# Kernel optimization log

Measured on AMD Instinct MI355X. Metric: run time of the kernel, lower is better.

The kernel has to match this reference:

```python
import jax, jax.numpy as jnp
import numpy as np

HG, WG, DG = 16, 16, 8   # bilateral grid size
NP = 12                  # affine params per pixel (3x4)
DS = 256                 # input_downsample


def _resize_bilinear(x, oh, ow):
    # torch F.interpolate(mode='bilinear', align_corners=False)
    B, C, H, W = x.shape
    sy, sx = H / oh, W / ow
    ys = jnp.clip((jnp.arange(oh, dtype=x.dtype) + 0.5) * sy - 0.5, 0.0, H - 1)
    xs = jnp.clip((jnp.arange(ow, dtype=x.dtype) + 0.5) * sx - 0.5, 0.0, W - 1)
    y0 = jnp.floor(ys).astype(jnp.int32); y1 = jnp.minimum(y0 + 1, H - 1)
    x0 = jnp.floor(xs).astype(jnp.int32); x1 = jnp.minimum(x0 + 1, W - 1)
    wy = (ys - y0.astype(x.dtype))[None, None, :, None]
    wx = (xs - x0.astype(x.dtype))[None, None, None, :]
    top = x[:, :, y0, :] * (1 - wy) + x[:, :, y1, :] * wy      # [B,C,oh,W]
    return top[:, :, :, x0] * (1 - wx) + top[:, :, :, x1] * wx  # [B,C,oh,ow]


def _conv(x, w, b):
    y = jax.lax.conv_general_dilated(x, w, (1, 1), 'SAME',
                                     dimension_numbers=('NCHW', 'OIHW', 'NCHW'))
    return y + b[None, :, None, None]


def _slice(grid, guide):
    # grid [B,C,Hg,Wg,D], guide [B,H,W] in [0,1].
    # Equivalent to the per-depth grid_sample(align_corners=True, border) +
    # depth gather/lerp loop: one fused trilinear lookup per pixel.
    B, C, Hg, Wg, D = grid.shape
    H, W = guide.shape[1], guide.shape[2]
    ys = jnp.arange(H, dtype=grid.dtype) * ((Hg - 1) / (H - 1))
    xs = jnp.arange(W, dtype=grid.dtype) * ((Wg - 1) / (W - 1))
    y0 = jnp.floor(ys).astype(jnp.int32); y1 = jnp.minimum(y0 + 1, Hg - 1)
    x0 = jnp.floor(xs).astype(jnp.int32); x1 = jnp.minimum(x0 + 1, Wg - 1)
    wy = (ys - y0.astype(grid.dtype))[:, None]   # [H,1]
    wx = (xs - x0.astype(grid.dtype))[None, :]   # [1,W]
    d = guide * (D - 1)
    d0 = jnp.clip(jnp.floor(d), 0, D - 1).astype(jnp.int32)
    d1 = jnp.minimum(d0 + 1, D - 1)
    wd = jnp.clip(d - d0.astype(grid.dtype), 0.0, 1.0)  # [B,H,W]

    Y0, Y1 = y0[:, None], y1[:, None]
    X0, X1 = x0[None, :], x1[None, :]

    def per_b(g, d0b, d1b, wdb):
        def dlerp(yi, xi):
            # g[:, yi, xi, d] -> [C,H,W]; lerp over depth
            return (1 - wdb) * g[:, yi, xi, d0b] + wdb * g[:, yi, xi, d1b]
        return ((1 - wy) * (1 - wx) * dlerp(Y0, X0)
                + (1 - wy) * wx * dlerp(Y0, X1)
                + wy * (1 - wx) * dlerp(Y1, X0)
                + wy * wx * dlerp(Y1, X1))

    return jax.vmap(per_b)(grid, d0, d1, wd)  # [B,C,H,W]


def _forward(x, w1, b1, w2, b2, w3, b3, w4, b4, w5, b5, w6, b6):
    B, C, H, W = x.shape
    guide = jnp.clip(0.299 * x[:, 0] + 0.587 * x[:, 1] + 0.114 * x[:, 2], 0.0, 1.0)
    scale = min(1.0, DS / max(H, W))
    if scale < 1.0:
        x_low = _resize_bilinear(x, int(H * scale), int(W * scale))
    else:
        x_low = x
    f = jax.nn.relu(_conv(x_low, w1, b1))
    f = jax.nn.relu(_conv(f, w2, b2))
    f = jax.nn.relu(_conv(f, w3, b3))
    c = jax.nn.relu(_conv(f, w4, b4))
    c = jax.nn.relu(_conv(c, w5, b5))
    c = _conv(c, w6, b6)                        # [B, NP*DG, H_low, W_low]
    c = _resize_bilinear(c, HG, WG)             # [B, NP*DG, HG, WG]
    grid = c.reshape(B, NP, DG, HG, WG).transpose(0, 1, 3, 4, 2)  # [B,NP,HG,WG,DG]
    sc = _slice(grid, guide)                    # [B, NP, H, W]
    co = sc.reshape(B, 3, 4, H, W)
    y = jnp.einsum('bijhw,bjhw->bihw', co[:, :, :3], x) + co[:, :, 3]
    return jnp.clip(y, 0.0, 1.0)


def setup_inputs() -> dict:
    key = jax.random.key(0)
    ks = jax.random.split(key, 7)
    x = jax.random.uniform(ks[0], (2, 3, 1024, 1024), dtype=jnp.float32)
    def wmat(k, o, i):
        return jax.random.normal(k, (o, i, 3, 3), jnp.float32) / np.sqrt(i * 9.0)
    return dict(
        x=x,
        w1=wmat(ks[1], 16, 3), b1=jnp.zeros((16,), jnp.float32),
        w2=wmat(ks[2], 32, 16), b2=jnp.zeros((32,), jnp.float32),
        w3=wmat(ks[3], 32, 32), b3=jnp.zeros((32,), jnp.float32),
        w4=wmat(ks[4], 64, 32), b4=jnp.zeros((64,), jnp.float32),
        w5=wmat(ks[5], 64, 64), b5=jnp.zeros((64,), jnp.float32),
        w6=wmat(ks[6], 96, 64), b6=jnp.zeros((96,), jnp.float32),
    )


def reference(x, w1, b1, w2, b2, w3, b3, w4, b4, w5, b5, w6, b6):
    return _forward(x, w1, b1, w2, b2, w3, b3, w4, b4, w5, b5, w6, b6)
```

## Files before the change

kernel.cpp:

```cpp
#include <hip/hip_runtime.h>
#include <hip/hip_bf16.h>

#define HW1K  1048576

typedef float  f4    __attribute__((ext_vector_type(4)));
typedef float  f32x4 __attribute__((ext_vector_type(4)));
typedef short  s16x8 __attribute__((ext_vector_type(8)));
typedef unsigned short u16x8 __attribute__((ext_vector_type(8)));

__device__ __forceinline__ float bf2f(unsigned short u) {
    unsigned int b = ((unsigned int)u) << 16;
    return __builtin_bit_cast(float, b);
}
__device__ __forceinline__ void fsplit(float x, unsigned short& h, unsigned short& l) {
    unsigned int xb = __builtin_bit_cast(unsigned int, x);
    h = (unsigned short)(xb >> 16);
    float fh = __builtin_bit_cast(float, xb & 0xffff0000u);
    float r = x - fh;
    l = (unsigned short)(__builtin_bit_cast(unsigned int, r) >> 16);
}

__global__ __launch_bounds__(256)
void prep_wM(const float* __restrict__ w2, const float* __restrict__ w3,
             const float* __restrict__ w4, const float* __restrict__ w5,
             const float* __restrict__ w6,
             unsigned short* __restrict__ Wh, unsigned short* __restrict__ Wl) {
    int i = blockIdx.x * 256 + threadIdx.x;
    if (i >= 124928) return;
    const float* src; int base, cin, kp_;
    if      (i < 5120)  { src = w2; base = 0;     cin = 16; kp_ = 160; }
    else if (i < 14336) { src = w3; base = 5120;  cin = 32; kp_ = 288; }
    else if (i < 32768) { src = w4; base = 14336; cin = 32; kp_ = 288; }
    else if (i < 69632) { src = w5; base = 32768; cin = 64; kp_ = 576; }
    else                { src = w6; base = 69632; cin = 64; kp_ = 576; }
    int r  = i - base;
    int co = r / kp_;
    int kp = r % kp_;
    int kk = kp / cin;
    int ci = kp % cin;
    float v = (kk < 9) ? src[(co * cin + ci) * 9 + kk] : 0.0f;
    unsigned short h, l; fsplit(v, h, l);
    Wh[i] = h; Wl[i] = l;
}

template <int WIN, int CIN, int COUT, int KP, int SO, int HOIST>
__device__ __forceinline__ void layerM(const unsigned short* sH, const unsigned short* sL,
                                       unsigned short* dH, unsigned short* dL,
                                       const unsigned short* __restrict__ Wh,
                                       const unsigned short* __restrict__ Wl,
                                       const float* __restrict__ bias) {
    constexpr int WOUT = WIN - 2;
    constexpr int NPX  = WOUT * WOUT;
    constexpr int CINP = CIN + 8;
    constexpr int MT   = (NPX + 15) / 16;
    constexpr int NT   = COUT / 16;
    constexpr int WPN  = 4 / NT;
    constexpr int KS   = KP / 32;

    const int wid  = threadIdx.x >> 6;
    const int lane = threadIdx.x & 63;
    const int m    = lane & 15;
    const int g    = lane >> 4;

    const int nt    = wid % NT;
    const int chunk = wid / NT;
    const int co    = nt * 16 + m;

    const unsigned short* wbh = Wh + (size_t)co * KP + 8 * g;
    const unsigned short* wbl = Wl + (size_t)co * KP + 8 * g;

    s16x8 bH[HOIST ? KS : 1], bL[HOIST ? KS : 1];
    if constexpr (HOIST) {
        #pragma unroll
        for (int k0 = 0; k0 < KS; ++k0) {
            bH[k0] = *(const s16x8*)(wbh + k0 * 32);
            bL[k0] = *(const s16x8*)(wbl + k0 * 32);
        }
    }
    const float bv = bias[co];

    #pragma unroll 1
    for (int mt = chunk; mt < MT; mt += WPN) {
        const int mt0 = mt * 16;
        int px = mt0 + m; if (px > NPX - 1) px = NPX - 1;
        const int pbase = (px / WOUT) * WIN + (px % WOUT);

        f32x4 aHH = {0,0,0,0}, aHL = {0,0,0,0}, aLH = {0,0,0,0};
        #pragma unroll
        for (int k0 = 0; k0 < KS; ++k0) {
            const int k   = k0 * 32 + 8 * g;
            const int kk  = k / CIN;
            const int ci0 = k % CIN;
            const int aoff = (pbase + (kk / 3) * WIN + (kk % 3)) * CINP + ci0;
            s16x8 avh = *(const s16x8*)(&sH[aoff]);
            s16x8 avl = *(const s16x8*)(&sL[aoff]);
            s16x8 bvh, bvl;
            if constexpr (HOIST) { bvh = bH[k0]; bvl = bL[k0]; }
            else {
                bvh = *(const s16x8*)(wbh + k0 * 32);
                bvl = *(const s16x8*)(wbl + k0 * 32);
            }
            aHH = __builtin_amdgcn_mfma_f32_16x16x32_bf16(avh, bvh, aHH, 0, 0, 0);
            aHL = __builtin_amdgcn_mfma_f32_16x16x32_bf16(avh, bvl, aHL, 0, 0, 0);
            aLH = __builtin_amdgcn_mfma_f32_16x16x32_bf16(avl, bvh, aLH, 0, 0, 0);
        }
        #pragma unroll
        for (int j = 0; j < 4; ++j) {
            int opx = mt0 + g * 4 + j;
            if (opx < NPX) {
                float v = fmaxf(aHH[j] + aHL[j] + aLH[j] + bv, 0.0f);
                unsigned short h, l; fsplit(v, h, l);
                dH[opx * SO + co] = h;
                dL[opx * SO + co] = l;
            }
        }
    }
}

__global__ __launch_bounds__(256, 3)
void fusedM(const float* __restrict__ x, const float* __restrict__ w1,
            const float* __restrict__ b1,
            const unsigned short* __restrict__ Wh, const unsigned short* __restrict__ Wl,
            const float* __restrict__ b2, const float* __restrict__ b3,
            const float* __restrict__ b4, const float* __restrict__ b5,
            unsigned short* __restrict__ P6h, unsigned short* __restrict__ P6l) {
    __shared__ float sC[592];
    __shared__ __align__(16) unsigned short AH[3840], AL[3840];
    __shared__ __align__(16) unsigned short BH[4000], BL[4000];

    const int cell = blockIdx.x;
    const int b = cell >> 8, gy = (cell >> 4) & 15, gx = cell & 15;

    for (int i = threadIdx.x; i < 588; i += 256) {
        int c = i / 196, t = i % 196;
        int xi = t % 14, yi = t / 14;
        int ya = 16 * gy + 1 + yi, xa = 16 * gx + 1 + xi;
        const float* p = x + ((size_t)(b * 3 + c)) * HW1K + (4 * ya + 1) * 1024 + (4 * xa + 1);
        sC[i] = 0.25f * (p[0] + p[1] + p[1024] + p[1025]);
    }
    for (int i = threadIdx.x; i < 384; i += 256) { AH[3456 + i] = 0; AL[3456 + i] = 0; }
    __syncthreads();

    {
        const int wid  = __builtin_amdgcn_readfirstlane(threadIdx.x >> 6);
        const int lane = threadIdx.x & 63;
        const int co0  = wid * 4;
        float acc[3][4]; int pxs[3], pb[3];
        #pragma unroll
        for (int t = 0; t < 3; ++t) {
            int px = lane + t * 64; if (px > 143) px = 143;
            pxs[t] = px; pb[t] = (px / 12) * 14 + (px % 12);
            #pragma unroll
            for (int j = 0; j < 4; ++j) acc[t][j] = b1[co0 + j];
        }
        for (int ci = 0; ci < 3; ++ci)
            #pragma unroll
            for (int k = 0; k < 9; ++k) {
                float w[4];
                #pragma unroll
                for (int j = 0; j < 4; ++j) w[j] = w1[((co0 + j) * 3 + ci) * 9 + k];
                const int ko = (k / 3) * 14 + (k % 3);
                #pragma unroll
                for (int t = 0; t < 3; ++t) {
                    float a = sC[ci * 196 + pb[t] + ko];
                    #pragma unroll
                    for (int j = 0; j < 4; ++j) acc[t][j] = fmaf(w[j], a, acc[t][j]);
                }
            }
        #pragma unroll
        for (int t = 0; t < 3; ++t)
            #pragma unroll
            for (int j = 0; j < 4; ++j) {
                float v = fmaxf(acc[t][j], 0.0f);
                unsigned short h, l; fsplit(v, h, l);
                AH[pxs[t] * 24 + co0 + j] = h;
                AL[pxs[t] * 24 + co0 + j] = l;
            }
    }
    __syncthreads();

    layerM<12, 16, 32, 160, 40, 1>(AH, AL, BH, BL, Wh + 0,     Wl + 0,     b2);
    __syncthreads();
    layerM<10, 32, 32, 288, 40, 1>(BH, BL, AH, AL, Wh + 5120,  Wl + 5120,  b3);
    __syncthreads();
    layerM< 8, 32, 64, 288, 72, 1>(AH, AL, BH, BL, Wh + 14336, Wl + 14336, b4);
    __syncthreads();
    layerM< 6, 64, 64, 576, 72, 0>(BH, BL, AH, AL, Wh + 32768, Wl + 32768, b5);
    __syncthreads();

    for (int t = threadIdx.x; t < 576; t += 256) {
        int kk = t >> 6, ci = t & 63;
        int ky = kk / 3, kx = kk % 3;
        float v = 0.0f;
        #pragma unroll
        for (int dr = 0; dr < 2; ++dr)
            #pragma unroll
            for (int dc = 0; dc < 2; ++dc) {
                int px = (ky + dr) * 4 + (kx + dc);
                v += bf2f(AH[px * 72 + ci]) + bf2f(AL[px * 72 + ci]);
            }
        v *= 0.25f;
        unsigned short h, l; fsplit(v, h, l);
        P6h[(size_t)cell * 576 + t] = h;
        P6l[(size_t)cell * 576 + t] = l;
    }
}

__global__ __launch_bounds__(64)
void gemm6(const unsigned short* __restrict__ Bh, const unsigned short* __restrict__ Bl,
           const unsigned short* __restrict__ W6h, const unsigned short* __restrict__ W6l,
           const float* __restrict__ b6, float* __restrict__ c16) {
    const int cell0 = blockIdx.x * 16;
    const int co0   = blockIdx.y * 16;
    const int lane  = threadIdx.x;
    const int m = lane & 15, g = lane >> 4;

    const unsigned short* pah = Bh  + (size_t)(cell0 + m) * 576 + 8 * g;
    const unsigned short* pal = Bl  + (size_t)(cell0 + m) * 576 + 8 * g;
    const unsigned short* pbh = W6h + (size_t)(co0 + m) * 576 + 8 * g;
    const unsigned short* pbl = W6l + (size_t)(co0 + m) * 576 + 8 * g;

    f32x4 aHH = {0,0,0,0}, aHL = {0,0,0,0}, aLH = {0,0,0,0};
    #pragma unroll 6
    for (int k0 = 0; k0 < 576; k0 += 32) {
        s16x8 avh = *(const s16x8*)(pah + k0);
        s16x8 avl = *(const s16x8*)(pal + k0);
        s16x8 bvh = *(const s16x8*)(pbh + k0);
        s16x8 bvl = *(const s16x8*)(pbl + k0);
        aHH = __builtin_amdgcn_mfma_f32_16x16x32_bf16(avh, bvh, aHH, 0, 0, 0);
        aHL = __builtin_amdgcn_mfma_f32_16x16x32_bf16(avh, bvl, aHL, 0, 0, 0);
        aLH = __builtin_amdgcn_mfma_f32_16x16x32_bf16(avl, bvh, aLH, 0, 0, 0);
    }
    const int co = co0 + m;
    const float bv = b6[co];
    #pragma unroll
    for (int j = 0; j < 4; ++j) {
        int cell = cell0 + g * 4 + j;
        float v = aHH[j] + aHL[j] + aLH[j] + bv;
        int b = cell >> 8, gyx = cell & 255;
        c16[(size_t)b * 24576 + (gyx * 8 + (co & 7)) * 12 + (co >> 3)] = v;
    }
}

__global__ __launch_bounds__(256)
void slice_apply4(const float* __restrict__ x, const float* __restrict__ c16,
                  float* __restrict__ out) {
    int t = blockIdx.x * 256 + threadIdx.x;
    int po4 = t * 4;
    int b   = po4 >> 20;
    int po  = po4 & (HW1K - 1);
    int py  = po >> 10;
    int px0 = po & 1023;

    const float* xb = x + (size_t)b * 3 * HW1K;
    f4 rv  = *(const f4*)(xb + po);
    f4 gv  = *(const f4*)(xb + HW1K + po);
    f4 bv  = *(const f4*)(xb + 2 * HW1K + po);

    float ysf = (float)py * (15.0f / 1023.0f);
    int y0 = (int)floorf(ysf); int y1 = min(y0 + 1, 15);
    float wy = ysf - (float)y0;

    const float* gb = c16 + (size_t)b * 24576;
    f4 outv[3];

    #pragma unroll
    for (int s = 0; s < 4; ++s) {
        float r  = rv[s], g = gv[s], bl = bv[s];
        int   px = px0 + s;

        float gd = fminf(fmaxf(0.299f * r + 0.587f * g + 0.114f * bl, 0.0f), 1.0f);

        float xsf = (float)px * (15.0f / 1023.0f);
        int x0 = (int)floorf(xsf); int x1 = min(x0 + 1, 15);
        float wx = xsf - (float)x0;

        float d  = gd * 7.0f;
        int d0 = (int)floorf(d); d0 = max(0, min(d0, 7));
        int d1 = min(d0 + 1, 7);
        float wd = fminf(fmaxf(d - (float)d0, 0.0f), 1.0f);

        float co[12];
        #pragma unroll
        for (int p = 0; p < 12; ++p) co[p] = 0.0f;

        #pragma unroll
        for (int cy = 0; cy < 2; ++cy) {
            int   yy  = cy ? y1 : y0;
            float wyf = cy ? wy : 1.0f - wy;
            #pragma unroll
            for (int cx = 0; cx < 2; ++cx) {
                int   xx  = cx ? x1 : x0;
                float wyx = wyf * (cx ? wx : 1.0f - wx);
                const float* g0 = gb + ((yy * 16 + xx) * 8 + d0) * 12;
                const float* g1 = gb + ((yy * 16 + xx) * 8 + d1) * 12;
                float wA = wyx * (1.0f - wd), wB = wyx * wd;
                #pragma unroll
                for (int p = 0; p < 12; ++p) co[p] += wA * g0[p] + wB * g1[p];
            }
        }

        #pragma unroll
        for (int i = 0; i < 3; ++i) {
            float v = co[i * 4 + 0] * r + co[i * 4 + 1] * g + co[i * 4 + 2] * bl + co[i * 4 + 3];
            outv[i][s] = fminf(fmaxf(v, 0.0f), 1.0f);
        }
    }

    float* ob = out + (size_t)b * 3 * HW1K;
    #pragma unroll
    for (int i = 0; i < 3; ++i)
        *(f4*)(ob + i * HW1K + po) = outv[i];
}

extern "C" void kernel_launch(void* const* d_in, const int* in_sizes, int n_in,
                              void* d_out, int out_size, void* d_ws, size_t ws_size,
                              hipStream_t stream) {
    const float* x  = (const float*)d_in[0];
    const float* w1 = (const float*)d_in[1];  const float* b1 = (const float*)d_in[2];
    const float* w2 = (const float*)d_in[3];  const float* b2 = (const float*)d_in[4];
    const float* w3 = (const float*)d_in[5];  const float* b3 = (const float*)d_in[6];
    const float* w4 = (const float*)d_in[7];  const float* b4 = (const float*)d_in[8];
    const float* w5 = (const float*)d_in[9];  const float* b5 = (const float*)d_in[10];
    const float* w6 = (const float*)d_in[11]; const float* b6 = (const float*)d_in[12];
    float* out = (float*)d_out;

    char* w = (char*)d_ws;
    unsigned short* Wh  = (unsigned short*)w;   w += 124928 * 2;
    unsigned short* Wl  = (unsigned short*)w;   w += 124928 * 2;
    unsigned short* P6h = (unsigned short*)w;   w += 512 * 576 * 2;
    unsigned short* P6l = (unsigned short*)w;   w += 512 * 576 * 2;
    float*          c16 = (float*)w;

    prep_wM<<<dim3(489),  dim3(256), 0, stream>>>(w2, w3, w4, w5, w6, Wh, Wl);
    fusedM <<<dim3(512),  dim3(256), 0, stream>>>(x, w1, b1, Wh, Wl, b2, b3, b4, b5, P6h, P6l);
    gemm6  <<<dim3(32, 6), dim3(64), 0, stream>>>(P6h, P6l, Wh + 69632, Wl + 69632, b6, c16);
    slice_apply4<<<dim3(2 * HW1K / 4 / 256), dim3(256), 0, stream>>>(x, c16, out);

    (void)in_sizes; (void)n_in; (void)out_size; (void)ws_size;
}
```

Baseline: 66.67 us.

## Double fusedM block to 512 threads, splitting layer work across 8 waves

Launches the fused conv kernel with 8 waves per block instead of 4, so each MFMA layer splits output tiles across twice as many waves (WPN doubled). The first conv layer is restructured so waves split pixel slices as well as output channels. This aims to hide latency within each of the 512 cells, since there are only 512 blocks. The cost is more register pressure per block (launch bounds become 512,2) and the extra waves may sit idle in small layers.

Result: slower. 71.73 us (+7.6%).

```diff
diff --git a/kernel.cpp b/kernel.cpp
--- a/kernel.cpp
+++ b/kernel.cpp
@@ -54,7 +54,7 @@
     constexpr int CINP = CIN + 8;
     constexpr int MT   = (NPX + 15) / 16;
     constexpr int NT   = COUT / 16;
-    constexpr int WPN  = 4 / NT;
+    constexpr int WPN  = 8 / NT;
     constexpr int KS   = KP / 32;
 
     const int wid  = threadIdx.x >> 6;
@@ -117,7 +117,7 @@
     }
 }
 
-__global__ __launch_bounds__(256, 3)
+__global__ __launch_bounds__(512, 2)
 void fusedM(const float* __restrict__ x, const float* __restrict__ w1,
             const float* __restrict__ b1,
             const unsigned short* __restrict__ Wh, const unsigned short* __restrict__ Wl,
@@ -131,51 +131,46 @@
     const int cell = blockIdx.x;
     const int b = cell >> 8, gy = (cell >> 4) & 15, gx = cell & 15;
 
-    for (int i = threadIdx.x; i < 588; i += 256) {
+    for (int i = threadIdx.x; i < 588; i += 512) {
         int c = i / 196, t = i % 196;
         int xi = t % 14, yi = t / 14;
         int ya = 16 * gy + 1 + yi, xa = 16 * gx + 1 + xi;
         const float* p = x + ((size_t)(b * 3 + c)) * HW1K + (4 * ya + 1) * 1024 + (4 * xa + 1);
         sC[i] = 0.25f * (p[0] + p[1] + p[1024] + p[1025]);
     }
-    for (int i = threadIdx.x; i < 384; i += 256) { AH[3456 + i] = 0; AL[3456 + i] = 0; }
+    for (int i = threadIdx.x; i < 384; i += 512) { AH[3456 + i] = 0; AL[3456 + i] = 0; }
     __syncthreads();
 
     {
         const int wid  = __builtin_amdgcn_readfirstlane(threadIdx.x >> 6);
         const int lane = threadIdx.x & 63;
-        const int co0  = wid * 4;
-        float acc[3][4]; int pxs[3], pb[3];
-        #pragma unroll
-        for (int t = 0; t < 3; ++t) {
-            int px = lane + t * 64; if (px > 143) px = 143;
-            pxs[t] = px; pb[t] = (px / 12) * 14 + (px % 12);
+        const int co0  = (wid & 3) * 4;
+        const int s0   = wid >> 2;
+        #pragma unroll 1
+        for (int s = s0; s < 3; s += 2) {
+            int px = lane + s * 64; if (px > 143) px = 143;
+            const int pb = (px / 12) * 14 + (px % 12);
+            f4 acc;
             #pragma unroll
-            for (int j = 0; j < 4; ++j) acc[t][j] = b1[co0 + j];
-        }
-        for (int ci = 0; ci < 3; ++ci)
-            #pragma unroll
-            for (int k = 0; k < 9; ++k) {
-                float w[4];
+            for (int j = 0; j < 4; ++j) acc[j] = b1[co0 + j];
+            for (int ci = 0; ci < 3; ++ci)
                 #pragma unroll
-                for (int j = 0; j < 4; ++j) w[j] = w1[((co0 + j) * 3 + ci) * 9 + k];
-                const int ko = (k / 3) * 14 + (k % 3);
-                #pragma unroll
-                for (int t = 0; t < 3; ++t) {
-                    float a = sC[ci * 196 + pb[t] + ko];
+                for (int k = 0; k < 9; ++k) {
+                    float w[4];
                     #pragma unroll
-                    for (int j = 0; j < 4; ++j) acc[t][j] = fmaf(w[j], a, acc[t][j]);
+                    for (int j = 0; j < 4; ++j) w[j] = w1[((co0 + j) * 3 + ci) * 9 + k];
+                    float a = sC[ci * 196 + pb + (k / 3) * 14 + (k % 3)];
+                    #pragma unroll
+                    for (int j = 0; j < 4; ++j) acc[j] = fmaf(w[j], a, acc[j]);
                 }
-            }
-        #pragma unroll
-        for (int t = 0; t < 3; ++t)
             #pragma unroll
             for (int j = 0; j < 4; ++j) {
-                float v = fmaxf(acc[t][j], 0.0f);
+                float v = fmaxf(acc[j], 0.0f);
                 unsigned short h, l; fsplit(v, h, l);
-                AH[pxs[t] * 24 + co0 + j] = h;
-                AL[pxs[t] * 24 + co0 + j] = l;
-            }
+                AH[px * 24 + co0 + j] = h;
+                AL[px * 24 + co0 + j] = l;
+            }
+        }
     }
     __syncthreads();
 
@@ -188,7 +183,7 @@
     layerM< 6, 64, 64, 576, 72, 0>(BH, BL, AH, AL, Wh + 32768, Wl + 32768, b5);
     __syncthreads();
 
-    for (int t = threadIdx.x; t < 576; t += 256) {
+    for (int t = threadIdx.x; t < 576; t += 512) {
         int kk = t >> 6, ci = t & 63;
         int ky = kk / 3, kx = kk % 3;
         float v = 0.0f;
@@ -333,7 +328,7 @@
     float*          c16 = (float*)w;
 
     prep_wM<<<dim3(489),  dim3(256), 0, stream>>>(w2, w3, w4, w5, w6, Wh, Wl);
-    fusedM <<<dim3(512),  dim3(256), 0, stream>>>(x, w1, b1, Wh, Wl, b2, b3, b4, b5, P6h, P6l);
+    fusedM <<<dim3(512),  dim3(512), 0, stream>>>(x, w1, b1, Wh, Wl, b2, b3, b4, b5, P6h, P6l);
     gemm6  <<<dim3(32, 6), dim3(64), 0, stream>>>(P6h, P6l, Wh + 69632, Wl + 69632, b6, c16);
     slice_apply4<<<dim3(2 * HW1K / 4 / 256), dim3(256), 0, stream>>>(x, c16, out);
 
```
